# Optimization experiments

Hardware: AMD Instinct MI355X
Metric: run time of the kernel (lower is better)

The kernel has to match this reference:

```python
import jax, jax.numpy as jnp
import numpy as np


def setup_inputs() -> dict:
    key = jax.random.key(0)
    k1, k2, k3 = jax.random.split(key, 3)
    N, V, C, T, H, W = 8, 3, 24, 8, 128, 128
    pred = jax.random.normal(k1, (N, V, C, T, H, W), dtype=jnp.float32)
    mask_extreme = jax.random.randint(k2, (N, H, W), 0, 2, dtype=jnp.int32)
    vq_0 = jax.random.normal(k3, (1, C), dtype=jnp.float32)
    return {"pred": pred, "mask_extreme": mask_extreme, "vq_0": vq_0}


def reference(pred, mask_extreme, vq_0):
    # pred: (N, V, C, T, H, W); mask_extreme: (N, H, W) in {0,1}; vq_0: (1, C)
    N, V, C, T, H, W = pred.shape
    m = mask_extreme.astype(pred.dtype)[:, None, None, None, :, :]   # (N,1,1,1,H,W)
    w = 1.0 - m                                                      # weights, broadcastable to pred
    # Broadcast quantization code to (1,1,C,1,1,1); it is a constant target (no grad).
    vq = jax.lax.stop_gradient(vq_0)[None, :, :, None, None, None]   # (1,1,C,1,1,1)
    # In the original, masked positions get vq := pred.detach() so their L1 is 0;
    # multiplying by w (0 there) is mathematically identical, without materializing
    # the repeated tensors.
    num = jnp.sum(jnp.abs(pred - vq) * w)
    # sum(weights) over the full repeated (N,V,C,T,H,W) tensor = V*C*T * sum over (N,H,W)
    den = jnp.sum(w) * jnp.asarray(V * C * T, pred.dtype)
    return num / den
```

## Files before the change

kernel.cpp:

```cpp
#include <hip/hip_runtime.h>


#define HW        16384u
#define PER_N     9437184u
#define CDIM      24u
#define N4        18874368u
#define NBLOCKS   8192u
#define STRIDE    2097152u

__global__ void __launch_bounds__(256) partial_kernel(
        const float4* __restrict__ pred4,
        const int*    __restrict__ mask,
        const float*  __restrict__ vq,
        float2* __restrict__ partials) {
    const unsigned idx = blockIdx.x * 256u + threadIdx.x;
    const unsigned e0  = idx << 2;
    const unsigned hw  = e0 & (HW - 1u);
    float acc_n = 0.0f, acc_w = 0.0f;
    #pragma unroll
    for (unsigned k = 0; k < 9u; ++k) {
        const unsigned j = idx + k * STRIDE;
        const unsigned e = e0 + (k << 23);
        const unsigned n = e / PER_N;
        const unsigned c = (e >> 17) % CDIM;
        float4 p = pred4[j];
        int4 m = *(const int4*)(mask + n * HW + hw);
        float v = vq[c];
        float w0 = (float)(1 - m.x), w1 = (float)(1 - m.y);
        float w2 = (float)(1 - m.z), w3 = (float)(1 - m.w);
        acc_n += fabsf(p.x - v) * w0 + fabsf(p.y - v) * w1
               + fabsf(p.z - v) * w2 + fabsf(p.w - v) * w3;
        acc_w += w0 + w1 + w2 + w3;
    }
    #pragma unroll
    for (int o = 32; o > 0; o >>= 1) {
        acc_n += __shfl_down(acc_n, o, 64);
        acc_w += __shfl_down(acc_w, o, 64);
    }
    __shared__ float sa[4], sb[4];
    const int lane = threadIdx.x & 63;
    const int wid  = threadIdx.x >> 6;
    if (lane == 0) { sa[wid] = acc_n; sb[wid] = acc_w; }
    __syncthreads();
    if (threadIdx.x == 0) {
        partials[blockIdx.x] = make_float2(sa[0] + sa[1] + sa[2] + sa[3],
                                           sb[0] + sb[1] + sb[2] + sb[3]);
    }
}

__global__ void __launch_bounds__(1024) reduce_kernel(
        const float2* __restrict__ partials, float* __restrict__ out) {
    float acc_n = 0.0f, acc_w = 0.0f;
    #pragma unroll
    for (unsigned i = 0; i < NBLOCKS / 1024u; ++i) {
        float2 p = partials[threadIdx.x + i * 1024u];
        acc_n += p.x;
        acc_w += p.y;
    }
    #pragma unroll
    for (int o = 32; o > 0; o >>= 1) {
        acc_n += __shfl_down(acc_n, o, 64);
        acc_w += __shfl_down(acc_w, o, 64);
    }
    __shared__ float sa[16], sb[16];
    const int lane = threadIdx.x & 63;
    const int wid  = threadIdx.x >> 6;
    if (lane == 0) { sa[wid] = acc_n; sb[wid] = acc_w; }
    __syncthreads();
    if (threadIdx.x == 0) {
        float n = 0.0f, w = 0.0f;
        #pragma unroll
        for (int i = 0; i < 16; ++i) { n += sa[i]; w += sb[i]; }
        out[0] = n / w;
    }
}

extern "C" void kernel_launch(void* const* d_in, const int* in_sizes, int n_in,
                              void* d_out, int out_size, void* d_ws, size_t ws_size,
                              hipStream_t stream) {
    const float* pred = (const float*)d_in[0];
    const int*   mask = (const int*)d_in[1];
    const float* vq   = (const float*)d_in[2];
    float2* partials = (float2*)d_ws;
    float*  out      = (float*)d_out;

    partial_kernel<<<NBLOCKS, 256, 0, stream>>>((const float4*)pred, mask, vq, partials);
    reduce_kernel<<<1, 1024, 0, stream>>>(partials, out);
}
```

Before: 394.3 us.

## Remap threads so each owns one (n,v,c) slab and reuses mask across T

Each thread now takes one fixed (n,v,c) group and a 4-pixel slice of H*W, then loops over the 8 T steps. The mask int4, the vq value and the weight sum are loaded and computed once per thread instead of once per loop step. This removes the per-iteration division and modulo index math and the repeated mask loads. Per-thread pred accesses within a step stay coalesced, and the block count grows to 9216 with 8 loads per thread instead of 9.

```diff
diff --git a/kernel.cpp b/kernel.cpp
--- a/kernel.cpp
+++ b/kernel.cpp
@@ -1,37 +1,40 @@
 #include <hip/hip_runtime.h>
 
 
-#define HW        16384u
-#define PER_N     9437184u
+#define HW4       16384u
+#define THW       131072u
 #define CDIM      24u
-#define N4        18874368u
-#define NBLOCKS   8192u
-#define STRIDE    2097152u
+#define VC        72u
+#define NTHREADS  2359296u
+#define NBLOCKS   9216u
+#define NPART     9216u
 
 __global__ void __launch_bounds__(256) partial_kernel(
         const float4* __restrict__ pred4,
         const int*    __restrict__ mask,
         const float*  __restrict__ vq,
         float2* __restrict__ partials) {
-    const unsigned idx = blockIdx.x * 256u + threadIdx.x;
-    const unsigned e0  = idx << 2;
-    const unsigned hw  = e0 & (HW - 1u);
-    float acc_n = 0.0f, acc_w = 0.0f;
+    const unsigned i = blockIdx.x * 256u + threadIdx.x;
+    const unsigned g = i >> 12;
+    const unsigned r = i & 4095u;
+    const unsigned n = g / VC;
+    const unsigned c = g % CDIM;
+    const float    v = vq[c];
+    const int4     m = *(const int4*)(mask + n * HW4 + r * 4u);
+    const float w0 = (float)(1 - m.x), w1 = (float)(1 - m.y);
+    const float w2 = (float)(1 - m.z), w3 = (float)(1 - m.w);
+    const float wsum8 = (w0 + w1 + w2 + w3) * 8.0f;
+
+    const unsigned j0 = g * (THW / 4u) + r;
+    float acc_n = 0.0f;
     #pragma unroll
-    for (unsigned k = 0; k < 9u; ++k) {
-        const unsigned j = idx + k * STRIDE;
-        const unsigned e = e0 + (k << 23);
-        const unsigned n = e / PER_N;
-        const unsigned c = (e >> 17) % CDIM;
-        float4 p = pred4[j];
-        int4 m = *(const int4*)(mask + n * HW + hw);
-        float v = vq[c];
-        float w0 = (float)(1 - m.x), w1 = (float)(1 - m.y);
-        float w2 = (float)(1 - m.z), w3 = (float)(1 - m.w);
+    for (unsigned k = 0; k < 8u; ++k) {
+        float4 p = pred4[j0 + k * (HW4 / 4u)];
         acc_n += fabsf(p.x - v) * w0 + fabsf(p.y - v) * w1
                + fabsf(p.z - v) * w2 + fabsf(p.w - v) * w3;
-        acc_w += w0 + w1 + w2 + w3;
     }
+    float acc_w = wsum8;
+
     #pragma unroll
     for (int o = 32; o > 0; o >>= 1) {
         acc_n += __shfl_down(acc_n, o, 64);
@@ -52,7 +55,7 @@
         const float2* __restrict__ partials, float* __restrict__ out) {
     float acc_n = 0.0f, acc_w = 0.0f;
     #pragma unroll
-    for (unsigned i = 0; i < NBLOCKS / 1024u; ++i) {
+    for (unsigned i = 0; i < NPART / 1024u; ++i) {
         float2 p = partials[threadIdx.x + i * 1024u];
         acc_n += p.x;
         acc_w += p.y;
```

New measurement: 389.2 us. About the same (-1.3%).
